# Optimization experiments

Hardware: AMD Instinct MI355X
Metric: run time of the kernel (lower is better)

## Reference

```python
import jax, jax.numpy as jnp
import numpy as np

N_NODES = 50000
N_EDGES = 800000
H = 128
D = 128
N_LAYERS = 4
N_GRAPHS = 128
NODE_VOCAB = 32
EDGE_VOCAB = 8
BN_EPS = 1e-5


def _bn(h, g, b):
    # BatchNorm1d, training-mode statistics (biased variance), as in the torch module
    m = h.mean(axis=0)
    v = ((h - m) ** 2).mean(axis=0)
    return (h - m) * jax.lax.rsqrt(v + BN_EPS) * g + b


def _gine(x, src, dst, e, eps_l):
    # GINEConv: message = ReLU(x_src + edge_attr), sum-aggregate at dst
    msg = jax.nn.relu(x[src] + e)                      # [E, H]
    aggr = jax.ops.segment_sum(msg, dst, num_segments=N_NODES)
    return (1.0 + eps_l) * x + aggr


def _forward(x_ids, edge_index, batch, edge_attr,
             node_emb, edge_emb, eps,
             init_W1, init_b1, init_g1, init_be1, init_W2, init_b2, init_g2, init_be2,
             mp_W1, mp_g1, mp_be1, mp_W2, mp_g2, mp_be2,
             l1_W1, l1_g1, l1_b1, l1_W2, l1_g2, l1_b2,
             l2_W1, l2_g1, l2_b1, l2_W2, l2_g2, l2_b2,
             fin_W):
    src, dst = edge_index[0], edge_index[1]
    x = node_emb[x_ids]                                # [N, H]
    e = edge_emb[edge_attr]                            # [E, H]
    # initialization conv (Linear layers WITH bias)
    h = _gine(x, src, dst, e, eps[0])
    h = jax.nn.relu(_bn(h @ init_W1 + init_b1, init_g1, init_be1))
    x = jax.nn.relu(_bn(h @ init_W2 + init_b2, init_g2, init_be2))
    # message-passing layers (Linear layers WITHOUT bias)
    for i in range(N_LAYERS):
        h = _gine(x, src, dst, e, eps[1 + i])
        h = jax.nn.relu(_bn(h @ mp_W1[i], mp_g1[i], mp_be1[i]))
        x = jax.nn.relu(_bn(h @ mp_W2[i], mp_g2[i], mp_be2[i]))
    # readout: global_add_pool
    g = jax.ops.segment_sum(x, batch, num_segments=N_GRAPHS)   # [G, H]
    # lin1 (outer F.relu is idempotent; dropout = identity in eval)
    h = jax.nn.relu(_bn(g @ l1_W1, l1_g1, l1_b1))
    h = jax.nn.relu(_bn(h @ l1_W2, l1_g2, l1_b2))
    # lin2
    h = jax.nn.relu(_bn(h @ l2_W1, l2_g1, l2_b1))
    h = jax.nn.relu(_bn(h @ l2_W2, l2_g2, l2_b2))
    return h @ fin_W                                   # [G, 1]


def setup_inputs() -> dict:
    key = jax.random.key(0)
    ks = jax.random.split(key, 20)
    s = 1.0 / np.sqrt(H)
    rn = lambda k, shp, sc: jax.random.normal(k, shp, dtype=jnp.float32) * sc
    return {
        "x_ids": jax.random.randint(ks[0], (N_NODES,), 0, NODE_VOCAB),
        "edge_index": jax.random.randint(ks[1], (2, N_EDGES), 0, N_NODES),
        "batch": jnp.sort(jax.random.randint(ks[2], (N_NODES,), 0, N_GRAPHS)),
        "edge_attr": jax.random.randint(ks[14], (N_EDGES,), 0, EDGE_VOCAB),
        "node_emb": rn(ks[3], (NODE_VOCAB, H), 0.05),
        "edge_emb": rn(ks[4], (EDGE_VOCAB, H), 0.05),
        "eps": jnp.zeros((N_LAYERS + 1,), jnp.float32),
        "init_W1": rn(ks[5], (H, D), s), "init_b1": jnp.zeros((D,)),
        "init_g1": jnp.ones((D,)), "init_be1": jnp.zeros((D,)),
        "init_W2": rn(ks[6], (D, H), s), "init_b2": jnp.zeros((H,)),
        "init_g2": jnp.ones((H,)), "init_be2": jnp.zeros((H,)),
        "mp_W1": rn(ks[7], (N_LAYERS, H, D), s),
        "mp_g1": jnp.ones((N_LAYERS, D)), "mp_be1": jnp.zeros((N_LAYERS, D)),
        "mp_W2": rn(ks[8], (N_LAYERS, D, H), s),
        "mp_g2": jnp.ones((N_LAYERS, H)), "mp_be2": jnp.zeros((N_LAYERS, H)),
        "l1_W1": rn(ks[9], (H, D), s), "l1_g1": jnp.ones((D,)), "l1_b1": jnp.zeros((D,)),
        "l1_W2": rn(ks[10], (D, D), s), "l1_g2": jnp.ones((D,)), "l1_b2": jnp.zeros((D,)),
        "l2_W1": rn(ks[11], (D, D), s), "l2_g1": jnp.ones((D,)), "l2_b1": jnp.zeros((D,)),
        "l2_W2": rn(ks[12], (D, H), s), "l2_g2": jnp.ones((H,)), "l2_b2": jnp.zeros((H,)),
        "fin_W": rn(ks[13], (H, 1), s),
    }


def reference(x_ids, edge_index, batch, edge_attr,
              node_emb, edge_emb, eps,
              init_W1, init_b1, init_g1, init_be1, init_W2, init_b2, init_g2, init_be2,
              mp_W1, mp_g1, mp_be1, mp_W2, mp_g2, mp_be2,
              l1_W1, l1_g1, l1_b1, l1_W2, l1_g2, l1_b2,
              l2_W1, l2_g1, l2_b1, l2_W2, l2_g2, l2_b2,
              fin_W):
    return _forward(x_ids, edge_index, batch, edge_attr,
                    node_emb, edge_emb, eps,
                    init_W1, init_b1, init_g1, init_be1, init_W2, init_b2, init_g2, init_be2,
                    mp_W1, mp_g1, mp_be1, mp_W2, mp_g2, mp_be2,
                    l1_W1, l1_g1, l1_b1, l1_W2, l1_g2, l1_b2,
                    l2_W1, l2_g1, l2_b1, l2_W2, l2_g2, l2_b2,
                    fin_W)
```

## Files before the change

### kernel.cpp

```cpp
#include <hip/hip_runtime.h>

#define NN 50000
#define NE 800000
#define NG 128
#define HD 128
#define NL 4
#define BN_EPS 1e-5f
#define REP 32
#define WP 136

typedef __attribute__((ext_vector_type(8))) short bf16x8;
typedef __attribute__((ext_vector_type(4))) float f32x4;

__device__ __forceinline__ unsigned short f2bf(float f) {
    unsigned u = __float_as_uint(f);
    u += 0x7FFFu + ((u >> 16) & 1u);
    return (unsigned short)(u >> 16);
}
__device__ __forceinline__ float bfval(unsigned short h) { return __uint_as_float((unsigned)h << 16); }
__device__ __forceinline__ float bflo(unsigned u) { return __uint_as_float(u << 16); }
__device__ __forceinline__ float bfhi(unsigned u) { return __uint_as_float(u & 0xFFFF0000u); }

__device__ __forceinline__ void split2(float a, float b, unsigned& hi, unsigned& lo) {
    unsigned ua = __float_as_uint(a), ub = __float_as_uint(b);
    hi = (ua >> 16) | (ub & 0xFFFF0000u);
    float ra = a - __uint_as_float(ua & 0xFFFF0000u);
    float rb = b - __uint_as_float(ub & 0xFFFF0000u);
    lo = (unsigned)f2bf(ra) | ((unsigned)f2bf(rb) << 16);
}
__device__ __forceinline__ unsigned pack2(float a, float b) {
    return (unsigned)f2bf(a) | ((unsigned)f2bf(b) << 16);
}

__device__ __forceinline__ void bn_pre(const float* SQbase,
                                       const float* gam, const float* bet,
                                       float inv_cnt, int t, float* scs, float* shs) {
    if (gam == nullptr) { scs[t] = 1.f; shs[t] = 0.f; return; }
    float s = 0.f, q = 0.f;
#pragma unroll
    for (int r = 0; r < REP; r++) {
        s += SQbase[r * 256 + t];
        q += SQbase[r * 256 + 128 + t];
    }
    float m = s * inv_cnt;
    float var = fmaxf(fmaf(q, inv_cnt, -m * m), 0.f);
    float inv = rsqrtf(var + BN_EPS);
    float sc = gam[t] * inv;
    scs[t] = sc;
    shs[t] = fmaf(-m, sc, bet[t]);
}

__global__ __launch_bounds__(256) void embed_kernel(const int* __restrict__ ids,
                                                    const float* __restrict__ emb,
                                                    unsigned short* __restrict__ Yb) {
    int i = blockIdx.x * 256 + threadIdx.x;
    if (i < NN * 16) {
        int node = i >> 4, g = i & 15;
        int id = ids[node];
        const float* p = emb + (size_t)id * HD + 8 * g;
        float4 a = *(const float4*)p;
        float4 b = *(const float4*)(p + 4);
        uint4 o;
        o.x = pack2(a.x, a.y); o.y = pack2(a.z, a.w);
        o.z = pack2(b.x, b.y); o.w = pack2(b.z, b.w);
        *(uint4*)(Yb + (size_t)node * HD + 8 * g) = o;
    }
}

__global__ __launch_bounds__(256) void ybn_kernel(const float* __restrict__ X,
                                                  const float* __restrict__ SQin,
                                                  const float* __restrict__ gam,
                                                  const float* __restrict__ bet,
                                                  unsigned short* __restrict__ Yb) {
    __shared__ float scs[HD], shs[HD];
    int t = threadIdx.x;
    if (t < HD) bn_pre(SQin, gam, bet, 1.f / NN, t, scs, shs);
    __syncthreads();
    int row = blockIdx.x * 16 + (t >> 4);
    int c8 = (t & 15) * 8;
    if (row < NN) {
        const float* p = X + (size_t)row * HD + c8;
        float4 v0 = *(const float4*)p;
        float4 v1 = *(const float4*)(p + 4);
        float4 s0 = *(const float4*)&scs[c8], s1 = *(const float4*)&scs[c8 + 4];
        float4 h0 = *(const float4*)&shs[c8], h1 = *(const float4*)&shs[c8 + 4];
        float f0 = fmaxf(fmaf(v0.x, s0.x, h0.x), 0.f), f1 = fmaxf(fmaf(v0.y, s0.y, h0.y), 0.f);
        float f2 = fmaxf(fmaf(v0.z, s0.z, h0.z), 0.f), f3 = fmaxf(fmaf(v0.w, s0.w, h0.w), 0.f);
        float f4 = fmaxf(fmaf(v1.x, s1.x, h1.x), 0.f), f5 = fmaxf(fmaf(v1.y, s1.y, h1.y), 0.f);
        float f6 = fmaxf(fmaf(v1.z, s1.z, h1.z), 0.f), f7 = fmaxf(fmaf(v1.w, s1.w, h1.w), 0.f);
        uint4 o;
        o.x = pack2(f0, f1); o.y = pack2(f2, f3);
        o.z = pack2(f4, f5); o.w = pack2(f6, f7);
        *(uint4*)(Yb + (size_t)row * HD + c8) = o;
    }
}

__global__ __launch_bounds__(256) void cvtw_kernel(const float* __restrict__ iw1,
                                                   const float* __restrict__ iw2,
                                                   const float* __restrict__ mw1,
                                                   const float* __restrict__ mw2,
                                                   unsigned short* __restrict__ Wh,
                                                   unsigned short* __restrict__ Wl) {
    int i = blockIdx.x * 256 + threadIdx.x;
    if (i >= 163840) return;
    int seg = i >> 14, loc = i & 16383;
    float v;
    if (seg == 0)      v = iw1[loc];
    else if (seg == 1) v = iw2[loc];
    else if (seg < 6)  v = mw1[(seg - 2) * 16384 + loc];
    else               v = mw2[(seg - 6) * 16384 + loc];
    int k = loc >> 7, n = loc & 127;
    unsigned short h = f2bf(v);
    float r = v - bfval(h);
    Wh[seg * 16384 + n * 128 + k] = h;
    Wl[seg * 16384 + n * 128 + k] = f2bf(r);
}

__global__ __launch_bounds__(256) void hist_kernel(const int* __restrict__ dst,
                                                   int* __restrict__ deg) {
    int e = blockIdx.x * 256 + threadIdx.x;
    if (e < NE) atomicAdd(&deg[dst[e]], 1);
}

__global__ __launch_bounds__(1024) void scan1_kernel(const int* __restrict__ deg,
                                                     int* __restrict__ rowptr,
                                                     int* __restrict__ blockSum) {
    __shared__ int s[1024];
    int b = blockIdx.x, t = threadIdx.x;
    int i = b * 1024 + t;
    int v = (i < NN) ? deg[i] : 0;
    s[t] = v;
    __syncthreads();
    for (int off = 1; off < 1024; off <<= 1) {
        int u = (t >= off) ? s[t - off] : 0;
        __syncthreads();
        s[t] += u;
        __syncthreads();
    }
    if (i < NN) rowptr[i] = s[t] - v;
    if (t == 1023) blockSum[b] = s[1023];
}

__global__ __launch_bounds__(64) void scan2_kernel(const int* __restrict__ blockSum,
                                                   int* __restrict__ blockOff,
                                                   int* __restrict__ rowptr, int nblocks) {
    int t = threadIdx.x;
    int orig = (t < nblocks) ? blockSum[t] : 0;
    int v = orig;
    for (int off = 1; off < 64; off <<= 1) {
        int u = __shfl_up(v, off, 64);
        if (t >= off) v += u;
    }
    if (t < nblocks) blockOff[t] = v - orig;
    if (t == nblocks - 1) rowptr[NN] = v;
}

__global__ __launch_bounds__(1024) void scan3_kernel(int* __restrict__ rowptr,
                                                     int* __restrict__ cursor,
                                                     const int* __restrict__ blockOff) {
    int b = blockIdx.x, t = threadIdx.x;
    int i = b * 1024 + t;
    if (i < NN) {
        int r = rowptr[i] + blockOff[b];
        rowptr[i] = r;
        cursor[i] = r;
    }
}

__global__ __launch_bounds__(256) void scatter_kernel(const int* __restrict__ src,
                                                      const int* __restrict__ dst,
                                                      const int* __restrict__ attr,
                                                      int* __restrict__ cursor,
                                                      unsigned* __restrict__ csr) {
    int e = blockIdx.x * 256 + threadIdx.x;
    if (e < NE) {
        int d = dst[e];
        int pos = atomicAdd(&cursor[d], 1);
        csr[pos] = (unsigned)src[e] | ((unsigned)attr[e] << 16);
    }
}

__device__ __forceinline__ void gine_acc(const unsigned short* __restrict__ Yb,
                                         const float* __restrict__ elds,
                                         unsigned p, int cq, float mask, float* a) {
    uint4 q = *(const uint4*)(Yb + (size_t)(p & 0xFFFFu) * HD + 8 * cq);
    const float* ep = elds + (p >> 16) * HD + 8 * cq;
    float4 e0 = *(const float4*)ep;
    float4 e1 = *(const float4*)(ep + 4);
    a[0] += mask * fmaxf(bflo(q.x) + e0.x, 0.f);
    a[1] += mask * fmaxf(bfhi(q.x) + e0.y, 0.f);
    a[2] += mask * fmaxf(bflo(q.y) + e0.z, 0.f);
    a[3] += mask * fmaxf(bfhi(q.y) + e0.w, 0.f);
    a[4] += mask * fmaxf(bflo(q.z) + e1.x, 0.f);
    a[5] += mask * fmaxf(bfhi(q.z) + e1.y, 0.f);
    a[6] += mask * fmaxf(bflo(q.w) + e1.z, 0.f);
    a[7] += mask * fmaxf(bfhi(q.w) + e1.w, 0.f);
}

__global__ __launch_bounds__(256) void conv_kernel(const unsigned short* __restrict__ Yb,
                                                   const int* __restrict__ rowptr,
                                                   const unsigned* __restrict__ csr,
                                                   const float* __restrict__ edge_emb,
                                                   const float* __restrict__ eps, int layer,
                                                   unsigned short* __restrict__ Ah,
                                                   unsigned short* __restrict__ Al) {
    __shared__ float elds[8 * HD];
    int t = threadIdx.x;
    ((float4*)elds)[t] = ((const float4*)edge_emb)[t];
    __syncthreads();
    int wave = t >> 6, lane = t & 63;
    int node = blockIdx.x * 4 + wave;
    if (node >= NN) return;
    int sub = lane >> 4, cq = lane & 15;
    int lo = rowptr[node], hi = rowptr[node + 1];
    float a[8];
#pragma unroll
    for (int i = 0; i < 8; i++) a[i] = 0.f;
    for (int base = lo; base < hi; base += 64) {
        unsigned pl = 0;
        int cnt = hi - base; if (cnt > 64) cnt = 64;
        if (base + lane < hi) pl = csr[base + lane];
        int j = 0;
        for (; j + 16 <= cnt; j += 16) {
            unsigned pa = __shfl(pl, j + sub, 64);
            unsigned pb = __shfl(pl, j + 4 + sub, 64);
            unsigned pc = __shfl(pl, j + 8 + sub, 64);
            unsigned pd = __shfl(pl, j + 12 + sub, 64);
            gine_acc(Yb, elds, pa, cq, 1.f, a);
            gine_acc(Yb, elds, pb, cq, 1.f, a);
            gine_acc(Yb, elds, pc, cq, 1.f, a);
            gine_acc(Yb, elds, pd, cq, 1.f, a);
        }
        for (; j + 8 <= cnt; j += 8) {
            unsigned pa = __shfl(pl, j + sub, 64);
            unsigned pb = __shfl(pl, j + 4 + sub, 64);
            gine_acc(Yb, elds, pa, cq, 1.f, a);
            gine_acc(Yb, elds, pb, cq, 1.f, a);
        }
        for (; j < cnt; j += 4) {
            int je = j + sub;
            bool val = (je < cnt);
            unsigned p = __shfl(pl, val ? je : j, 64);
            gine_acc(Yb, elds, p, cq, val ? 1.f : 0.f, a);
        }
    }
#pragma unroll
    for (int i = 0; i < 8; i++) {
        a[i] += __shfl_xor(a[i], 16, 64);
        a[i] += __shfl_xor(a[i], 32, 64);
    }
    if (sub == 0) {
        float g = 1.f + eps[layer];
        uint4 q = *(const uint4*)(Yb + (size_t)node * HD + 8 * cq);
        float o0 = fmaf(g, bflo(q.x), a[0]), o1 = fmaf(g, bfhi(q.x), a[1]);
        float o2 = fmaf(g, bflo(q.y), a[2]), o3 = fmaf(g, bfhi(q.y), a[3]);
        float o4 = fmaf(g, bflo(q.z), a[4]), o5 = fmaf(g, bfhi(q.z), a[5]);
        float o6 = fmaf(g, bflo(q.w), a[6]), o7 = fmaf(g, bfhi(q.w), a[7]);
        uint4 H, L;
        split2(o0, o1, H.x, L.x);
        split2(o2, o3, H.y, L.y);
        split2(o4, o5, H.z, L.z);
        split2(o6, o7, H.w, L.w);
        *(uint4*)(Ah + (size_t)node * HD + 8 * cq) = H;
        *(uint4*)(Al + (size_t)node * HD + 8 * cq) = L;
    }
}

__global__ __launch_bounds__(256) void mm_mfma_pre(const unsigned short* __restrict__ Ah,
                                                   const unsigned short* __restrict__ Al,
                                                   const unsigned short* __restrict__ Wh,
                                                   const unsigned short* __restrict__ Wl,
                                                   const float* __restrict__ bias,
                                                   float* __restrict__ out,
                                                   float* __restrict__ SQout) {
    __shared__ unsigned short WhS[64 * WP];
    __shared__ unsigned short WlS[64 * WP];
    int t = threadIdx.x;
    int rowblk = blockIdx.x >> 1;
    int colbase = (blockIdx.x & 1) * 64;
    const unsigned short* sh = Wh + (size_t)colbase * HD;
    const unsigned short* sl = Wl + (size_t)colbase * HD;
#pragma unroll
    for (int i = 0; i < 4; i++) {
        int idx = t + i * 256;
        int col = idx >> 4, kk = (idx & 15) * 8;
        *(uint4*)(WhS + col * WP + kk) = *(const uint4*)(sh + (size_t)col * HD + kk);
        *(uint4*)(WlS + col * WP + kk) = *(const uint4*)(sl + (size_t)col * HD + kk);
    }
    __syncthreads();
    int w = t >> 6, lane = t & 63;
    int quad = lane >> 4, nl = lane & 15;
    int row0 = rowblk * 64 + w * 16;
    int rA = row0 + nl;
    bool ok = rA < NN;
    f32x4 acc[4];
#pragma unroll
    for (int i = 0; i < 4; i++) acc[i] = (f32x4){0.f, 0.f, 0.f, 0.f};
#pragma unroll
    for (int kc = 0; kc < 4; kc++) {
        int k0 = kc * 32 + quad * 8;
        bf16x8 ah = ok ? *(const bf16x8*)(Ah + (size_t)rA * HD + k0) : (bf16x8)0;
        bf16x8 al = ok ? *(const bf16x8*)(Al + (size_t)rA * HD + k0) : (bf16x8)0;
#pragma unroll
        for (int c = 0; c < 4; c++) {
            int wof = (c * 16 + nl) * WP + k0;
            bf16x8 bh = *(const bf16x8*)(WhS + wof);
            bf16x8 bl = *(const bf16x8*)(WlS + wof);
            acc[c] = __builtin_amdgcn_mfma_f32_16x16x32_bf16(ah, bh, acc[c], 0, 0, 0);
            acc[c] = __builtin_amdgcn_mfma_f32_16x16x32_bf16(al, bh, acc[c], 0, 0, 0);
            acc[c] = __builtin_amdgcn_mfma_f32_16x16x32_bf16(ah, bl, acc[c], 0, 0, 0);
        }
    }
    int rep = (blockIdx.x & (REP - 1)) * 256;
#pragma unroll
    for (int c = 0; c < 4; c++) {
        int col = colbase + c * 16 + nl;
        float bv = bias ? bias[col] : 0.f;
        f32x4 v = acc[c];
        float s = 0.f, qq = 0.f;
#pragma unroll
        for (int r = 0; r < 4; r++) {
            int grow = row0 + quad * 4 + r;
            float val = v[r] + bv;
            if (grow < NN) {
                out[(size_t)grow * HD + col] = val;
                s += val;
                qq += val * val;
            }
        }
        s += __shfl_xor(s, 16, 64);  s += __shfl_xor(s, 32, 64);
        qq += __shfl_xor(qq, 16, 64); qq += __shfl_xor(qq, 32, 64);
        if (quad == 0) {
            atomicAdd(&SQout[rep + col], s);
            atomicAdd(&SQout[rep + 128 + col], qq);
        }
    }
}

__global__ __launch_bounds__(256) void mm_mfma_act(const float* __restrict__ A,
                                                   const unsigned short* __restrict__ Wh,
                                                   const unsigned short* __restrict__ Wl,
                                                   const float* __restrict__ bias,
                                                   const float* __restrict__ SQin,
                                                   const float* __restrict__ gam,
                                                   const float* __restrict__ bet,
                                                   float* __restrict__ out,
                                                   float* __restrict__ SQout) {
    __shared__ unsigned short WhS[64 * WP];
    __shared__ unsigned short WlS[64 * WP];
    __shared__ float scs[HD], shs[HD];
    int t = threadIdx.x;
    int rowblk = blockIdx.x >> 1;
    int colbase = (blockIdx.x & 1) * 64;
    if (t < HD) bn_pre(SQin, gam, bet, 1.f / NN, t, scs, shs);
    const unsigned short* sh = Wh + (size_t)colbase * HD;
    const unsigned short* sl = Wl + (size_t)colbase * HD;
#pragma unroll
    for (int i = 0; i < 4; i++) {
        int idx = t + i * 256;
        int col = idx >> 4, kk = (idx & 15) * 8;
        *(uint4*)(WhS + col * WP + kk) = *(const uint4*)(sh + (size_t)col * HD + kk);
        *(uint4*)(WlS + col * WP + kk) = *(const uint4*)(sl + (size_t)col * HD + kk);
    }
    __syncthreads();
    int w = t >> 6, lane = t & 63;
    int quad = lane >> 4, nl = lane & 15;
    int row0 = rowblk * 64 + w * 16;
    int rA = row0 + nl;
    bool ok = rA < NN;
    f32x4 acc[4];
#pragma unroll
    for (int i = 0; i < 4; i++) acc[i] = (f32x4){0.f, 0.f, 0.f, 0.f};
#pragma unroll
    for (int kc = 0; kc < 4; kc++) {
        int k0 = kc * 32 + quad * 8;
        float4 s0 = *(const float4*)&scs[k0], s1 = *(const float4*)&scs[k0 + 4];
        float4 t0 = *(const float4*)&shs[k0], t1 = *(const float4*)&shs[k0 + 4];
        float4 v0 = ok ? *(const float4*)(A + (size_t)rA * HD + k0) : make_float4(0, 0, 0, 0);
        float4 v1 = ok ? *(const float4*)(A + (size_t)rA * HD + k0 + 4) : make_float4(0, 0, 0, 0);
        float f0 = fmaxf(fmaf(v0.x, s0.x, t0.x), 0.f), f1 = fmaxf(fmaf(v0.y, s0.y, t0.y), 0.f);
        float f2 = fmaxf(fmaf(v0.z, s0.z, t0.z), 0.f), f3 = fmaxf(fmaf(v0.w, s0.w, t0.w), 0.f);
        float f4 = fmaxf(fmaf(v1.x, s1.x, t1.x), 0.f), f5 = fmaxf(fmaf(v1.y, s1.y, t1.y), 0.f);
        float f6 = fmaxf(fmaf(v1.z, s1.z, t1.z), 0.f), f7 = fmaxf(fmaf(v1.w, s1.w, t1.w), 0.f);
        if (!ok) { f0 = f1 = f2 = f3 = f4 = f5 = f6 = f7 = 0.f; }
        unsigned h0, h1, h2, h3, l0, l1, l2, l3;
        split2(f0, f1, h0, l0); split2(f2, f3, h1, l1);
        split2(f4, f5, h2, l2); split2(f6, f7, h3, l3);
        bf16x8 ah = __builtin_bit_cast(bf16x8, make_uint4(h0, h1, h2, h3));
        bf16x8 al = __builtin_bit_cast(bf16x8, make_uint4(l0, l1, l2, l3));
#pragma unroll
        for (int c = 0; c < 4; c++) {
            int wof = (c * 16 + nl) * WP + k0;
            bf16x8 bh = *(const bf16x8*)(WhS + wof);
            bf16x8 bl = *(const bf16x8*)(WlS + wof);
            acc[c] = __builtin_amdgcn_mfma_f32_16x16x32_bf16(ah, bh, acc[c], 0, 0, 0);
            acc[c] = __builtin_amdgcn_mfma_f32_16x16x32_bf16(al, bh, acc[c], 0, 0, 0);
            acc[c] = __builtin_amdgcn_mfma_f32_16x16x32_bf16(ah, bl, acc[c], 0, 0, 0);
        }
    }
    int rep = (blockIdx.x & (REP - 1)) * 256;
#pragma unroll
    for (int c = 0; c < 4; c++) {
        int col = colbase + c * 16 + nl;
        float bv = bias ? bias[col] : 0.f;
        f32x4 v = acc[c];
        float s = 0.f, qq = 0.f;
#pragma unroll
        for (int r = 0; r < 4; r++) {
            int grow = row0 + quad * 4 + r;
            float val = v[r] + bv;
            if (grow < NN) {
                out[(size_t)grow * HD + col] = val;
                s += val;
                qq += val * val;
            }
        }
        s += __shfl_xor(s, 16, 64);  s += __shfl_xor(s, 32, 64);
        qq += __shfl_xor(qq, 16, 64); qq += __shfl_xor(qq, 32, 64);
        if (quad == 0) {
            atomicAdd(&SQout[rep + col], s);
            atomicAdd(&SQout[rep + 128 + col], qq);
        }
    }
}

__global__ __launch_bounds__(256) void readout_kernel(const float* __restrict__ x,
                                                      const int* __restrict__ batch,
                                                      const float* __restrict__ SQin,
                                                      const float* __restrict__ gam,
                                                      const float* __restrict__ bet,
                                                      float* __restrict__ gout) {
    __shared__ int bat[256];
    __shared__ float scs[HD], shs[HD];
    int t = threadIdx.x;
    int rq = t >> 5, cq = t & 31;
    int r0 = blockIdx.x * 256;
    int i = r0 + t;
    bat[t] = (i < NN) ? batch[i] : -1;
    if (t < HD) bn_pre(SQin, gam, bet, 1.f / NN, t, scs, shs);
    __syncthreads();
    float4 s4 = *(const float4*)&scs[4 * cq];
    float4 h4 = *(const float4*)&shs[4 * cq];
    float4 acc = make_float4(0.f, 0.f, 0.f, 0.f);
    int gcur = -1;
    for (int j = rq; j < 256; j += 8) {
        int r = r0 + j;
        if (r >= NN) break;
        int g = bat[j];
        if (g != gcur) {
            if (gcur >= 0) {
                atomicAdd(&gout[(size_t)gcur * HD + 4 * cq + 0], acc.x);
                atomicAdd(&gout[(size_t)gcur * HD + 4 * cq + 1], acc.y);
                atomicAdd(&gout[(size_t)gcur * HD + 4 * cq + 2], acc.z);
                atomicAdd(&gout[(size_t)gcur * HD + 4 * cq + 3], acc.w);
            }
            acc = make_float4(0.f, 0.f, 0.f, 0.f);
            gcur = g;
        }
        float4 v = *(const float4*)(x + (size_t)r * HD + 4 * cq);
        acc.x += fmaxf(fmaf(v.x, s4.x, h4.x), 0.f);
        acc.y += fmaxf(fmaf(v.y, s4.y, h4.y), 0.f);
        acc.z += fmaxf(fmaf(v.z, s4.z, h4.z), 0.f);
        acc.w += fmaxf(fmaf(v.w, s4.w, h4.w), 0.f);
    }
    if (gcur >= 0) {
        atomicAdd(&gout[(size_t)gcur * HD + 4 * cq + 0], acc.x);
        atomicAdd(&gout[(size_t)gcur * HD + 4 * cq + 1], acc.y);
        atomicAdd(&gout[(size_t)gcur * HD + 4 * cq + 2], acc.z);
        atomicAdd(&gout[(size_t)gcur * HD + 4 * cq + 3], acc.w);
    }
}

__global__ __launch_bounds__(256) void head_mm(const float* __restrict__ A,
                                               const float* __restrict__ W,
                                               const float* __restrict__ SQin,
                                               const float* __restrict__ gam,
                                               const float* __restrict__ bet,
                                               float* __restrict__ out,
                                               float* __restrict__ SQout) {
    const int PADK = 132;
    __shared__ float As[64 * PADK];
    __shared__ float colS[HD], colQ[HD];
    __shared__ float scs[HD], shs[HD];
    int t = threadIdx.x;
    if (t < HD) {
        colS[t] = 0.f; colQ[t] = 0.f;
        bn_pre(SQin, gam, bet, 1.f / NG, t, scs, shs);
    }
    __syncthreads();
    int row0 = blockIdx.x * 64;
#pragma unroll
    for (int i = 0; i < 8; i++) {
        int idx = t + i * 256;
        int r = idx >> 5, kq = idx & 31;
        float4 v = *(const float4*)(A + (size_t)(row0 + r) * HD + 4 * kq);
        float4 s4 = *(const float4*)&scs[4 * kq];
        float4 h4 = *(const float4*)&shs[4 * kq];
        v.x = fmaxf(fmaf(v.x, s4.x, h4.x), 0.f);
        v.y = fmaxf(fmaf(v.y, s4.y, h4.y), 0.f);
        v.z = fmaxf(fmaf(v.z, s4.z, h4.z), 0.f);
        v.w = fmaxf(fmaf(v.w, s4.w, h4.w), 0.f);
        *(float4*)&As[r * PADK + 4 * kq] = v;
    }
    __syncthreads();
    int jq = t & 31, rb = t >> 5;
    float acc[8][4];
#pragma unroll
    for (int i = 0; i < 8; i++)
#pragma unroll
        for (int j = 0; j < 4; j++) acc[i][j] = 0.f;
    const float* Wp = W + 4 * jq;
    const float* Ap = &As[rb * 8 * PADK];
    for (int k = 0; k < HD; k += 4) {
        float4 w0 = *(const float4*)(Wp + (size_t)(k + 0) * HD);
        float4 w1 = *(const float4*)(Wp + (size_t)(k + 1) * HD);
        float4 w2 = *(const float4*)(Wp + (size_t)(k + 2) * HD);
        float4 w3 = *(const float4*)(Wp + (size_t)(k + 3) * HD);
#pragma unroll
        for (int i = 0; i < 8; i++) {
            float4 a4 = *(const float4*)&Ap[i * PADK + k];
            acc[i][0] = fmaf(a4.x, w0.x, acc[i][0]);
            acc[i][1] = fmaf(a4.x, w0.y, acc[i][1]);
            acc[i][2] = fmaf(a4.x, w0.z, acc[i][2]);
            acc[i][3] = fmaf(a4.x, w0.w, acc[i][3]);
            acc[i][0] = fmaf(a4.y, w1.x, acc[i][0]);
            acc[i][1] = fmaf(a4.y, w1.y, acc[i][1]);
            acc[i][2] = fmaf(a4.y, w1.z, acc[i][2]);
            acc[i][3] = fmaf(a4.y, w1.w, acc[i][3]);
            acc[i][0] = fmaf(a4.z, w2.x, acc[i][0]);
            acc[i][1] = fmaf(a4.z, w2.y, acc[i][1]);
            acc[i][2] = fmaf(a4.z, w2.z, acc[i][2]);
            acc[i][3] = fmaf(a4.z, w2.w, acc[i][3]);
            acc[i][0] = fmaf(a4.w, w3.x, acc[i][0]);
            acc[i][1] = fmaf(a4.w, w3.y, acc[i][1]);
            acc[i][2] = fmaf(a4.w, w3.z, acc[i][2]);
            acc[i][3] = fmaf(a4.w, w3.w, acc[i][3]);
        }
    }
    float s0 = 0, s1 = 0, s2 = 0, s3 = 0, q0 = 0, q1 = 0, q2 = 0, q3 = 0;
#pragma unroll
    for (int i = 0; i < 8; i++) {
        int gr = row0 + rb * 8 + i;
        float4 v = make_float4(acc[i][0], acc[i][1], acc[i][2], acc[i][3]);
        *(float4*)(out + (size_t)gr * HD + 4 * jq) = v;
        s0 += v.x; q0 += v.x * v.x;
        s1 += v.y; q1 += v.y * v.y;
        s2 += v.z; q2 += v.z * v.z;
        s3 += v.w; q3 += v.w * v.w;
    }
    atomicAdd(&colS[4 * jq + 0], s0); atomicAdd(&colQ[4 * jq + 0], q0);
    atomicAdd(&colS[4 * jq + 1], s1); atomicAdd(&colQ[4 * jq + 1], q1);
    atomicAdd(&colS[4 * jq + 2], s2); atomicAdd(&colQ[4 * jq + 2], q2);
    atomicAdd(&colS[4 * jq + 3], s3); atomicAdd(&colQ[4 * jq + 3], q3);
    __syncthreads();
    int rep = (blockIdx.x & (REP - 1)) * 256;
    if (t < HD) {
        atomicAdd(&SQout[rep + t], colS[t]);
        atomicAdd(&SQout[rep + 128 + t], colQ[t]);
    }
}

__global__ __launch_bounds__(128) void final_kernel(const float* __restrict__ h,
                                                    const float* __restrict__ SQin,
                                                    const float* __restrict__ gam,
                                                    const float* __restrict__ bet,
                                                    const float* __restrict__ finW,
                                                    float* __restrict__ out) {
    __shared__ float scs[HD], shs[HD];
    int t = threadIdx.x;
    bn_pre(SQin, gam, bet, 1.f / NG, t, scs, shs);
    __syncthreads();
    float s = 0.f;
    for (int c = 0; c < HD; c++) {
        float v = h[(size_t)t * HD + c];
        v = fmaxf(fmaf(v, scs[c], shs[c]), 0.f);
        s += v * finW[c];
    }
    out[t] = s;
}

extern "C" void kernel_launch(void* const* d_in, const int* in_sizes, int n_in,
                              void* d_out, int out_size, void* d_ws, size_t ws_size,
                              hipStream_t stream) {
    const int* x_ids = (const int*)d_in[0];
    const int* edge_index = (const int*)d_in[1];
    const int* batch = (const int*)d_in[2];
    const int* edge_attr = (const int*)d_in[3];
    const float* node_emb = (const float*)d_in[4];
    const float* edge_emb = (const float*)d_in[5];
    const float* eps = (const float*)d_in[6];
    const float* init_W1 = (const float*)d_in[7];
    const float* init_b1 = (const float*)d_in[8];
    const float* init_g1 = (const float*)d_in[9];
    const float* init_be1 = (const float*)d_in[10];
    const float* init_W2 = (const float*)d_in[11];
    const float* init_b2 = (const float*)d_in[12];
    const float* init_g2 = (const float*)d_in[13];
    const float* init_be2 = (const float*)d_in[14];
    const float* mp_W1 = (const float*)d_in[15];
    const float* mp_g1 = (const float*)d_in[16];
    const float* mp_be1 = (const float*)d_in[17];
    const float* mp_W2 = (const float*)d_in[18];
    const float* mp_g2 = (const float*)d_in[19];
    const float* mp_be2 = (const float*)d_in[20];
    const float* l1_W1 = (const float*)d_in[21];
    const float* l1_g1 = (const float*)d_in[22];
    const float* l1_b1 = (const float*)d_in[23];
    const float* l1_W2 = (const float*)d_in[24];
    const float* l1_g2 = (const float*)d_in[25];
    const float* l1_b2 = (const float*)d_in[26];
    const float* l2_W1 = (const float*)d_in[27];
    const float* l2_g1 = (const float*)d_in[28];
    const float* l2_b1 = (const float*)d_in[29];
    const float* l2_W2 = (const float*)d_in[30];
    const float* l2_g2 = (const float*)d_in[31];
    const float* l2_b2 = (const float*)d_in[32];
    const float* fin_W = (const float*)d_in[33];

    const int* e_src = edge_index;
    const int* e_dst = edge_index + NE;

    const size_t STG = (size_t)REP * 256;
    float* ws = (float*)d_ws;
    float* X = ws;
    float* Bbuf = X + (size_t)NN * HD;
    unsigned short* Yb = (unsigned short*)Bbuf;
    unsigned short* Ah = (unsigned short*)(Bbuf + (size_t)NN * HD);
    unsigned short* Al = Ah + (size_t)NN * HD;
    float* Gp = (float*)(Al + (size_t)NN * HD);
    float* Hp = Gp + NG * HD;
    float* Hp2 = Hp + NG * HD;
    float* SQ = Hp2 + NG * HD;
    int* rowptr = (int*)(SQ + 14 * STG);
    int* cursor = rowptr + 50048;
    int* deg = cursor + 50048;
    int* blockSum = deg + 50048;
    int* blockOff = blockSum + 64;
    unsigned* csr = (unsigned*)(blockOff + 64);
    unsigned short* Wh = (unsigned short*)(csr + NE);
    unsigned short* Wl = Wh + 163840;

    hipMemsetAsync(deg, 0, NN * sizeof(int), stream);
    hipMemsetAsync(SQ, 0, 14 * STG * sizeof(float), stream);
    hipMemsetAsync(Gp, 0, NG * HD * sizeof(float), stream);

    const int SCAN_BLOCKS = (NN + 1023) / 1024;
    embed_kernel<<<(NN * 16 + 255) / 256, 256, 0, stream>>>(x_ids, node_emb, Yb);
    cvtw_kernel<<<640, 256, 0, stream>>>(init_W1, init_W2, mp_W1, mp_W2, Wh, Wl);
    hist_kernel<<<(NE + 255) / 256, 256, 0, stream>>>(e_dst, deg);
    scan1_kernel<<<SCAN_BLOCKS, 1024, 0, stream>>>(deg, rowptr, blockSum);
    scan2_kernel<<<1, 64, 0, stream>>>(blockSum, blockOff, rowptr, SCAN_BLOCKS);
    scan3_kernel<<<SCAN_BLOCKS, 1024, 0, stream>>>(rowptr, cursor, blockOff);
    scatter_kernel<<<(NE + 255) / 256, 256, 0, stream>>>(e_src, e_dst, edge_attr, cursor, csr);

    const int mfma_grid = ((NN + 63) / 64) * 2;
    const int ybn_grid = (NN + 15) / 16;
    for (int i = 0; i <= NL; i++) {
        const unsigned short* Wh1 = Wh + (size_t)(i == 0 ? 0 : 2 + (i - 1)) * 16384;
        const unsigned short* Wl1 = Wl + (size_t)(i == 0 ? 0 : 2 + (i - 1)) * 16384;
        const unsigned short* Wh2 = Wh + (size_t)(i == 0 ? 1 : 6 + (i - 1)) * 16384;
        const unsigned short* Wl2 = Wl + (size_t)(i == 0 ? 1 : 6 + (i - 1)) * 16384;
        const float* b1 = (i == 0) ? init_b1 : nullptr;
        const float* b2 = (i == 0) ? init_b2 : nullptr;
        const float* g1 = (i == 0) ? init_g1 : mp_g1 + (size_t)(i - 1) * HD;
        const float* be1 = (i == 0) ? init_be1 : mp_be1 + (size_t)(i - 1) * HD;
        const float* gp = (i == 1) ? init_g2 : mp_g2 + (size_t)(i - 2) * HD;
        const float* bp = (i == 1) ? init_be2 : mp_be2 + (size_t)(i - 2) * HD;
        float* Sprev = SQ + (size_t)(2 * i - 1) * STG;
        float* S1 = SQ + (size_t)(2 * i) * STG;
        float* S2 = SQ + (size_t)(2 * i + 1) * STG;

        if (i > 0) ybn_kernel<<<ybn_grid, 256, 0, stream>>>(X, Sprev, gp, bp, Yb);
        conv_kernel<<<(NN + 3) / 4, 256, 0, stream>>>(Yb, rowptr, csr, edge_emb, eps, i, Ah, Al);
        mm_mfma_pre<<<mfma_grid, 256, 0, stream>>>(Ah, Al, Wh1, Wl1, b1, Bbuf, S1);
        mm_mfma_act<<<mfma_grid, 256, 0, stream>>>(Bbuf, Wh2, Wl2, b2, S1, g1, be1, X, S2);
    }

    float* S9 = SQ + 9 * STG;
    readout_kernel<<<(NN + 255) / 256, 256, 0, stream>>>(
        X, batch, S9, mp_g2 + 3 * HD, mp_be2 + 3 * HD, Gp);

    float* S10 = SQ + 10 * STG;
    float* S11 = SQ + 11 * STG;
    float* S12 = SQ + 12 * STG;
    float* S13 = SQ + 13 * STG;
    head_mm<<<2, 256, 0, stream>>>(Gp, l1_W1, nullptr, nullptr, nullptr, Hp, S10);
    head_mm<<<2, 256, 0, stream>>>(Hp, l1_W2, S10, l1_g1, l1_b1, Hp2, S11);
    head_mm<<<2, 256, 0, stream>>>(Hp2, l2_W1, S11, l1_g2, l1_b2, Hp, S12);
    head_mm<<<2, 256, 0, stream>>>(Hp, l2_W2, S12, l2_g1, l2_b1, Hp2, S13);
    final_kernel<<<1, 128, 0, stream>>>(Hp2, S13, l2_g2, l2_b2, fin_W, (float*)d_out);
}
```

Before: 801.9 us.

## Replace global-atomic CSR scatter with two-pass bucketed binning

```diff
diff --git a/kernel.cpp b/kernel.cpp
--- a/kernel.cpp
+++ b/kernel.cpp
@@ -8,6 +8,8 @@
 #define BN_EPS 1e-5f
 #define REP 32
 #define WP 136
+#define NB 392
+#define EPB 4096
 
 typedef __attribute__((ext_vector_type(8))) short bf16x8;
 typedef __attribute__((ext_vector_type(4))) float f32x4;
@@ -157,26 +159,89 @@
 
 __global__ __launch_bounds__(1024) void scan3_kernel(int* __restrict__ rowptr,
                                                      int* __restrict__ cursor,
-                                                     const int* __restrict__ blockOff) {
+                                                     const int* __restrict__ blockOff,
+                                                     int* __restrict__ bucketCursor) {
     int b = blockIdx.x, t = threadIdx.x;
     int i = b * 1024 + t;
     if (i < NN) {
         int r = rowptr[i] + blockOff[b];
         rowptr[i] = r;
         cursor[i] = r;
-    }
-}
-
-__global__ __launch_bounds__(256) void scatter_kernel(const int* __restrict__ src,
-                                                      const int* __restrict__ dst,
-                                                      const int* __restrict__ attr,
-                                                      int* __restrict__ cursor,
-                                                      unsigned* __restrict__ csr) {
-    int e = blockIdx.x * 256 + threadIdx.x;
-    if (e < NE) {
-        int d = dst[e];
-        int pos = atomicAdd(&cursor[d], 1);
-        csr[pos] = (unsigned)src[e] | ((unsigned)attr[e] << 16);
+        if ((i & 127) == 0) bucketCursor[i >> 7] = r;
+    }
+}
+
+__global__ __launch_bounds__(256) void bin_kernel(const int* __restrict__ src,
+                                                  const int* __restrict__ dst,
+                                                  const int* __restrict__ attr,
+                                                  int* __restrict__ bucketCursor,
+                                                  uint2* __restrict__ ebuf) {
+    __shared__ int cnt[512];
+    __shared__ int sc[512], sc2[512];
+    __shared__ int base[512];
+    __shared__ int garr[NB];
+    __shared__ int wof[NB];
+    __shared__ uint2 stage[EPB];
+    int t = threadIdx.x;
+    int e0 = blockIdx.x * EPB;
+    for (int i = t; i < 512; i += 256) cnt[i] = 0;
+    __syncthreads();
+    int myb[16]; unsigned myv[16]; int myd[16];
+#pragma unroll
+    for (int j = 0; j < 16; j++) {
+        int e = e0 + t + j * 256;
+        if (e < NE) {
+            int d = dst[e];
+            myd[j] = d;
+            myv[j] = (unsigned)src[e] | ((unsigned)attr[e] << 16);
+            myb[j] = d >> 7;
+            atomicAdd(&cnt[myb[j]], 1);
+        } else myb[j] = -1;
+    }
+    __syncthreads();
+    for (int k = t; k < 512; k += 256) sc[k] = cnt[k];
+    __syncthreads();
+    int* sp = sc; int* dp = sc2;
+    for (int off = 1; off < 512; off <<= 1) {
+        for (int k = t; k < 512; k += 256) dp[k] = sp[k] + (k >= off ? sp[k - off] : 0);
+        __syncthreads();
+        int* tmp = sp; sp = dp; dp = tmp;
+    }
+    for (int k = t; k < 512; k += 256) base[k] = sp[k] - cnt[k];
+    int total = sp[511];
+    __syncthreads();
+    for (int b = t; b < NB; b += 256) {
+        wof[b] = 0;
+        if (b < 512 && cnt[b] > 0) garr[b] = atomicAdd(&bucketCursor[b], cnt[b]);
+    }
+    __syncthreads();
+#pragma unroll
+    for (int j = 0; j < 16; j++) {
+        if (myb[j] >= 0) {
+            int slot = base[myb[j]] + atomicAdd(&wof[myb[j]], 1);
+            stage[slot] = make_uint2(myv[j], (unsigned)myd[j]);
+        }
+    }
+    __syncthreads();
+    for (int i = t; i < total; i += 256) {
+        uint2 u = stage[i];
+        int b = (int)(u.y >> 7);
+        ebuf[garr[b] + (i - base[b])] = u;
+    }
+}
+
+__global__ __launch_bounds__(256) void place_kernel(const uint2* __restrict__ ebuf,
+                                                    const int* __restrict__ rowptr,
+                                                    int* __restrict__ cursor,
+                                                    unsigned* __restrict__ csr) {
+    int b = blockIdx.x;
+    int n0 = b * 128;
+    int n1 = n0 + 128; if (n1 > NN) n1 = NN;
+    int es = rowptr[n0], ee = rowptr[n1];
+    for (int i = es + threadIdx.x; i < ee; i += 256) {
+        uint2 u = ebuf[i];
+        int pos = atomicAdd(&cursor[u.y], 1);
+        csr[pos] = u.x;
     }
 }
 
@@ -636,9 +701,11 @@
     int* deg = cursor + 50048;
     int* blockSum = deg + 50048;
     int* blockOff = blockSum + 64;
-    unsigned* csr = (unsigned*)(blockOff + 64);
+    int* bucketCursor = blockOff + 64;
+    unsigned* csr = (unsigned*)(bucketCursor + NB);
     unsigned short* Wh = (unsigned short*)(csr + NE);
     unsigned short* Wl = Wh + 163840;
+    uint2* ebuf = (uint2*)(Wl + 163840);
 
     hipMemsetAsync(deg, 0, NN * sizeof(int), stream);
     hipMemsetAsync(SQ, 0, 14 * STG * sizeof(float), stream);
@@ -650,8 +717,10 @@
     hist_kernel<<<(NE + 255) / 256, 256, 0, stream>>>(e_dst, deg);
     scan1_kernel<<<SCAN_BLOCKS, 1024, 0, stream>>>(deg, rowptr, blockSum);
     scan2_kernel<<<1, 64, 0, stream>>>(blockSum, blockOff, rowptr, SCAN_BLOCKS);
-    scan3_kernel<<<SCAN_BLOCKS, 1024, 0, stream>>>(rowptr, cursor, blockOff);
-    scatter_kernel<<<(NE + 255) / 256, 256, 0, stream>>>(e_src, e_dst, edge_attr, cursor, csr);
+    scan3_kernel<<<SCAN_BLOCKS, 1024, 0, stream>>>(rowptr, cursor, blockOff, bucketCursor);
+    bin_kernel<<<(NE + EPB - 1) / EPB, 256, 0, stream>>>(e_src, e_dst, edge_attr,
+                                                         bucketCursor, ebuf);
+    place_kernel<<<(NN + 127) / 128, 256, 0, stream>>>(ebuf, rowptr, cursor, csr);
 
     const int mfma_grid = ((NN + 63) / 64) * 2;
     const int ybn_grid = (NN + 15) / 16;
```

Result: faster. 786.0 us (-2.0%).
